# Kernel tuning notes

Measured on AMD Instinct MI355X. Metric: run time of the kernel, lower is better.

## Reference

```python
import jax, jax.numpy as jnp
import numpy as np

HIDDEN = 1024
HEADS = 16
HEAD_DIM = HIDDEN // HEADS
SCALE = float(np.sqrt(HEAD_DIM))


def setup_inputs() -> dict:
    key = jax.random.key(0)
    ks = jax.random.split(key, 9)
    B, S = 2, 2048
    x = jax.random.normal(ks[0], (B, S, HIDDEN), dtype=jnp.float32)
    mask = jnp.ones((B, S, S), dtype=jnp.int32)
    init = 1.0 / np.sqrt(HIDDEN)
    def lin(k):
        kw, kb = jax.random.split(k)
        W = jax.random.uniform(kw, (HIDDEN, HIDDEN), jnp.float32, -init, init)
        b = jax.random.uniform(kb, (HIDDEN,), jnp.float32, -init, init)
        return W, b
    Wq, bq = lin(ks[1])
    Wk, bk = lin(ks[2])
    Wv, bv = lin(ks[3])
    Wo, bo = lin(ks[4])
    return {"x": x, "mask": mask, "Wq": Wq, "bq": bq, "Wk": Wk, "bk": bk,
            "Wv": Wv, "bv": bv, "Wo": Wo, "bo": bo}


def reference(x, mask, Wq, bq, Wk, bk, Wv, bv, Wo, bo):
    B, S, _ = x.shape
    # Linear projections, split into heads: [B, H, S, Dh]
    def proj(W, b):
        y = jnp.einsum('bsd,ed->bse', x, W) + b  # torch Linear: x @ W.T + b
        return y.reshape(B, S, HEADS, HEAD_DIM).transpose(0, 2, 1, 3)
    q = proj(Wq, bq)
    k = proj(Wk, bk)
    v = proj(Wv, bv)
    scores = jnp.einsum('bhqd,bhkd->bhqk', q, k) / SCALE  # [B,H,S,S]
    scores = jnp.where(mask[:, None, :, :] == 0, jnp.float32(-1e9), scores)
    attn = jax.nn.softmax(scores, axis=-1)
    # dropout is identity at inference (eval mode)
    out = jnp.einsum('bhqk,bhkd->bhqd', attn, v)
    out = out.transpose(0, 2, 1, 3).reshape(B, S, HIDDEN)
    return jnp.einsum('bsd,ed->bse', out, Wo) + bo
```

## Files before the change

kernel.cpp:

```cpp
#include <hip/hip_runtime.h>
#include <hip/hip_bf16.h>

typedef __attribute__((ext_vector_type(8))) short bf16x8;
typedef __attribute__((ext_vector_type(4))) float f32x4;
typedef __attribute__((ext_vector_type(16))) float f32x16;
typedef unsigned int uint;

typedef __attribute__((address_space(1))) void as1_void;
typedef __attribute__((address_space(3))) void as3_void;

__device__ __forceinline__ void gload16(const void* g, void* l) {
  __builtin_amdgcn_global_load_lds((as1_void*)(void*)g, (as3_void*)l, 16, 0, 0);
}

__device__ __forceinline__ f32x4 mfma16(bf16x8 a, bf16x8 b, f32x4 c) {
  return __builtin_amdgcn_mfma_f32_16x16x32_bf16(a, b, c, 0, 0, 0);
}

__device__ __forceinline__ f32x16 mfma32(bf16x8 a, bf16x8 b, f32x16 c) {
  return __builtin_amdgcn_mfma_f32_32x32x16_bf16(a, b, c, 0, 0, 0);
}

__global__ __launch_bounds__(256) void castf2b(const float* __restrict__ s,
                                               __hip_bfloat16* __restrict__ d, int n) {
  int i = (blockIdx.x * 256 + threadIdx.x) * 4;
  if (i >= n) return;
  float4 f = *reinterpret_cast<const float4*>(s + i);
  union { __hip_bfloat16 h[4]; uint2 u; } cv;
  cv.h[0] = __float2bfloat16(f.x);
  cv.h[1] = __float2bfloat16(f.y);
  cv.h[2] = __float2bfloat16(f.z);
  cv.h[3] = __float2bfloat16(f.w);
  *reinterpret_cast<uint2*>(d + i) = cv.u;
}

__global__ __launch_bounds__(256) void castw(
    const float* __restrict__ Wq, const float* __restrict__ Wk,
    const float* __restrict__ Wv, const float* __restrict__ Wo,
    __hip_bfloat16* __restrict__ wqkv, __hip_bfloat16* __restrict__ wo) {
  int seg = blockIdx.x >> 10;
  int i = ((blockIdx.x & 1023) * 256 + threadIdx.x) * 4;
  const float* s = seg == 0 ? Wq : seg == 1 ? Wk : seg == 2 ? Wv : Wo;
  __hip_bfloat16* d = seg < 3 ? wqkv + seg * 1048576 : wo;
  float4 f = *reinterpret_cast<const float4*>(s + i);
  union { __hip_bfloat16 h[4]; uint2 u; } cv;
  cv.h[0] = __float2bfloat16(f.x);
  cv.h[1] = __float2bfloat16(f.y);
  cv.h[2] = __float2bfloat16(f.z);
  cv.h[3] = __float2bfloat16(f.w);
  *reinterpret_cast<uint2*>(d + i) = cv.u;
}

__global__ __launch_bounds__(256) void mask_pack(const int* __restrict__ m,
                                                 unsigned long long* __restrict__ bits) {
  int g = blockIdx.x * 256 + threadIdx.x;
  unsigned long long bal = __ballot(m[g] != 0);
  if ((threadIdx.x & 63) == 0) bits[g >> 6] = bal;
}

__global__ __launch_bounds__(256) void vtrans(const __hip_bfloat16* __restrict__ v,
                                              __hip_bfloat16* __restrict__ vt) {
  int bh = blockIdx.x >> 5;
  int s0 = (blockIdx.x & 31) * 64;
  __shared__ __align__(16) __hip_bfloat16 tile[64][72];
  const __hip_bfloat16* src = v + ((size_t)bh * 2048 + s0) * 64;
  int t = threadIdx.x;
#pragma unroll
  for (int i = 0; i < 2; i++) {
    int c = t + i * 256;
    int r = c >> 3, c8 = (c & 7) * 8;
    *reinterpret_cast<uint4*>(&tile[r][c8]) =
        *reinterpret_cast<const uint4*>(src + (size_t)r * 64 + c8);
  }
  __syncthreads();
  __hip_bfloat16* dst = vt + (size_t)bh * 64 * 2048 + s0;
#pragma unroll
  for (int i = 0; i < 2; i++) {
    int c = t + i * 256;
    int d = c >> 3, s8 = (c & 7) * 8;
    __hip_bfloat16 tmp[8] __attribute__((aligned(16)));
#pragma unroll
    for (int j = 0; j < 8; j++) tmp[j] = tile[s8 + j][d];
    *reinterpret_cast<uint4*>(dst + (size_t)d * 2048 + s8) =
        *reinterpret_cast<const uint4*>(tmp);
  }
}

template <int MODE>
__global__ __launch_bounds__(256) void gemm_bt(
    const __hip_bfloat16* __restrict__ A, const __hip_bfloat16* __restrict__ Bw,
    const float* __restrict__ bias0, const float* __restrict__ bias1,
    const float* __restrict__ bias2, __hip_bfloat16* __restrict__ out0,
    __hip_bfloat16* __restrict__ out1, __hip_bfloat16* __restrict__ out2,
    float* __restrict__ foutp, int M, int N, int K) {
  __shared__ __align__(16) __hip_bfloat16 Alds[128 * 64];
  __shared__ __align__(16) __hip_bfloat16 Blds[128 * 64];
  const int t = threadIdx.x;
  const int lane = t & 63;
  const int w = t >> 6;
  const int wr = w >> 1, wc = w & 1;
  const int l15 = lane & 15, lhi = lane >> 4;
  const int Nt = N >> 7;
  const int bm = (int)blockIdx.x / Nt, bn = (int)blockIdx.x % Nt;
  const int m0 = bm * 128, n0 = bn * 128;

  const f32x4 fzero = {0.f, 0.f, 0.f, 0.f};
  f32x4 acc[4][4];
#pragma unroll
  for (int mi = 0; mi < 4; mi++)
#pragma unroll
    for (int ni = 0; ni < 4; ni++) acc[mi][ni] = fzero;

  for (int k0 = 0; k0 < K; k0 += 64) {
#pragma unroll
    for (int i = 0; i < 4; i++) {
      int c = t + i * 256;
      int r = c >> 3, c8 = (c & 7) * 8;
      gload16(A + (size_t)(m0 + r) * K + k0 + c8, (char*)Alds + c * 16);
      gload16(Bw + (size_t)(n0 + r) * K + k0 + c8, (char*)Blds + c * 16);
    }
    __syncthreads();
#pragma unroll
    for (int kk = 0; kk < 2; kk++) {
      bf16x8 af[4], bfr[4];
#pragma unroll
      for (int mi = 0; mi < 4; mi++)
        af[mi] = *reinterpret_cast<const bf16x8*>(
            &Alds[(wr * 64 + mi * 16 + l15) * 64 + kk * 32 + lhi * 8]);
#pragma unroll
      for (int ni = 0; ni < 4; ni++)
        bfr[ni] = *reinterpret_cast<const bf16x8*>(
            &Blds[(wc * 64 + ni * 16 + l15) * 64 + kk * 32 + lhi * 8]);
#pragma unroll
      for (int mi = 0; mi < 4; mi++)
#pragma unroll
        for (int ni = 0; ni < 4; ni++)
          acc[mi][ni] = mfma16(af[mi], bfr[ni], acc[mi][ni]);
    }
    __syncthreads();
  }

#pragma unroll
  for (int mi = 0; mi < 4; mi++) {
#pragma unroll
    for (int ni = 0; ni < 4; ni++) {
#pragma unroll
      for (int r = 0; r < 4; r++) {
        int gr = m0 + wr * 64 + mi * 16 + lhi * 4 + r;
        int gc = n0 + wc * 64 + ni * 16 + l15;
        float v = acc[mi][ni][r];
        if (MODE == 0) {
          int seg = gc >> 10, e = gc & 1023, h = e >> 6, d = e & 63;
          int b = gr >> 11, s = gr & 2047;
          size_t idx = (((size_t)(b * 16 + h)) * 2048 + s) * 64 + d;
          if (seg == 0)
            out0[idx] = __float2bfloat16((v + bias0[e]) * 0.125f);
          else if (seg == 1)
            out1[idx] = __float2bfloat16(v + bias1[e]);
          else
            out2[idx] = __float2bfloat16(v + bias2[e]);
        } else {
          foutp[(size_t)gr * N + gc] = v + bias0[gc];
        }
      }
    }
  }
}

__global__ __launch_bounds__(256) void attn2(
    const __hip_bfloat16* __restrict__ Q, const __hip_bfloat16* __restrict__ Kk,
    const __hip_bfloat16* __restrict__ VT,
    const unsigned long long* __restrict__ mb, __hip_bfloat16* __restrict__ ctx) {
  int bx = blockIdx.x;
  int bid = (bx & 7) * 128 + (bx >> 3);
  int bh = bid >> 5, qc = bid & 31;
  int b = bh >> 4, h = bh & 15;
  int lane = threadIdx.x & 63, w = threadIdx.x >> 6;
  int l31 = lane & 31, lh = lane >> 5, lh4 = lh * 4;
  int wsb = w & 1;
  int kvh = w >> 1;
  int q0 = qc * 64 + wsb * 32;
  int kvbase = kvh * 1024;

  __shared__ float olds[2][32][64];
  __shared__ float mlds[2][2][32];
  __shared__ float llds[2][2][32];

  const __hip_bfloat16* Qrow = Q + ((size_t)bh * 2048 + q0 + l31) * 64 + lh * 8;
  const __hip_bfloat16* Krow =
      Kk + ((size_t)bh * 2048 + kvbase + l31) * 64 + lh * 8;
  const __hip_bfloat16* V0 =
      VT + ((size_t)bh * 64 + l31) * 2048 + kvbase + lh * 8;
  const __hip_bfloat16* V1 = V0 + 32 * 2048;
  const unsigned long long* Mrow =
      mb + ((size_t)b * 2048 + q0 + l31) * 32 + kvh * 16;

  bf16x8 qf[4];
#pragma unroll
  for (int ck = 0; ck < 4; ck++)
    qf[ck] = *reinterpret_cast<const bf16x8*>(Qrow + ck * 16);

  f32x16 o0 = {}, o1 = {};
  float mrun = -3.0e38f, lrun = 0.f;

  unsigned long long mw = Mrow[0], mwn = 0;
  bool skipm = __all(mw == ~0ull);

  auto comp = [&](const bf16x8* kf, const bf16x8* vf, int sh) {
    f32x16 s = {};
#pragma unroll
    for (int ck = 0; ck < 4; ck++) s = mfma32(kf[ck], qf[ck], s);
    if (!skipm) {
      uint mh = (uint)(mw >> sh) >> lh4;
#pragma unroll
      for (int r = 0; r < 16; r++) {
        int cr = (r & 3) + 8 * (r >> 2);
        if (!((mh >> cr) & 1u)) s[r] = -1e9f;
      }
    }
    float pmax = s[0];
#pragma unroll
    for (int r = 1; r < 16; r++) pmax = fmaxf(pmax, s[r]);
    pmax = fmaxf(pmax, __shfl_xor(pmax, 32));
    if (!__all(pmax <= mrun + 8.0f)) {
      float nm = fmaxf(mrun, pmax);
      float scl = __expf(mrun - nm);
      mrun = nm;
      lrun *= scl;
#pragma unroll
      for (int r = 0; r < 16; r++) {
        int cr = (r & 3) + 8 * (r >> 2);
        float sr = __shfl(scl, cr + lh4);
        o0[r] *= sr;
        o1[r] *= sr;
      }
    }
    float p[16];
    float ts = 0.f;
#pragma unroll
    for (int r = 0; r < 16; r++) {
      p[r] = __expf(s[r] - mrun);
      ts += p[r];
    }
    ts += __shfl_xor(ts, 32);
    lrun += ts;
    uint x0, x1, x2, x3, y0, y1, y2, y3;
    asm("v_cvt_pk_bf16_f32 %0, %1, %2" : "=v"(x0) : "v"(p[0]), "v"(p[1]));
    asm("v_cvt_pk_bf16_f32 %0, %1, %2" : "=v"(y0) : "v"(p[4]), "v"(p[5]));
    asm("v_cvt_pk_bf16_f32 %0, %1, %2" : "=v"(x1) : "v"(p[2]), "v"(p[3]));
    asm("v_cvt_pk_bf16_f32 %0, %1, %2" : "=v"(y1) : "v"(p[6]), "v"(p[7]));
    asm("v_cvt_pk_bf16_f32 %0, %1, %2" : "=v"(x2) : "v"(p[8]), "v"(p[9]));
    asm("v_cvt_pk_bf16_f32 %0, %1, %2" : "=v"(y2) : "v"(p[12]), "v"(p[13]));
    asm("v_cvt_pk_bf16_f32 %0, %1, %2" : "=v"(x3) : "v"(p[10]), "v"(p[11]));
    asm("v_cvt_pk_bf16_f32 %0, %1, %2" : "=v"(y3) : "v"(p[14]), "v"(p[15]));
    asm volatile("v_permlane32_swap_b32 %0, %1" : "+v"(x0), "+v"(y0));
    asm volatile("v_permlane32_swap_b32 %0, %1" : "+v"(x1), "+v"(y1));
    asm volatile("v_permlane32_swap_b32 %0, %1" : "+v"(x2), "+v"(y2));
    asm volatile("v_permlane32_swap_b32 %0, %1" : "+v"(x3), "+v"(y3));
    union { uint u[4]; bf16x8 v8; } pa0, pa1;
    pa0.u[0] = x0; pa0.u[1] = x1; pa0.u[2] = y0; pa0.u[3] = y1;
    pa1.u[0] = x2; pa1.u[1] = x3; pa1.u[2] = y2; pa1.u[3] = y3;
    o0 = mfma32(pa0.v8, vf[0], o0);
    o0 = mfma32(pa1.v8, vf[1], o0);
    o1 = mfma32(pa0.v8, vf[2], o1);
    o1 = mfma32(pa1.v8, vf[3], o1);
  };

  bf16x8 kfA[4], vfA[4], kfB[4], vfB[4];
#pragma unroll
  for (int ck = 0; ck < 4; ck++)
    kfA[ck] = *reinterpret_cast<const bf16x8*>(Krow + ck * 16);
  vfA[0] = *reinterpret_cast<const bf16x8*>(V0);
  vfA[1] = *reinterpret_cast<const bf16x8*>(V0 + 16);
  vfA[2] = *reinterpret_cast<const bf16x8*>(V1);
  vfA[3] = *reinterpret_cast<const bf16x8*>(V1 + 16);

  for (int i = 0; i < 16; ++i) {
    const int t1 = 2 * i + 1;
#pragma unroll
    for (int ck = 0; ck < 4; ck++)
      kfB[ck] = *reinterpret_cast<const bf16x8*>(Krow + t1 * 2048 + ck * 16);
    vfB[0] = *reinterpret_cast<const bf16x8*>(V0 + t1 * 32);
    vfB[1] = *reinterpret_cast<const bf16x8*>(V0 + t1 * 32 + 16);
    vfB[2] = *reinterpret_cast<const bf16x8*>(V1 + t1 * 32);
    vfB[3] = *reinterpret_cast<const bf16x8*>(V1 + t1 * 32 + 16);
    mwn = Mrow[i + 1 < 16 ? i + 1 : 15];

    comp(kfA, vfA, 0);

    if (i < 15) {
      const int t2 = 2 * i + 2;
#pragma unroll
      for (int ck = 0; ck < 4; ck++)
        kfA[ck] = *reinterpret_cast<const bf16x8*>(Krow + t2 * 2048 + ck * 16);
      vfA[0] = *reinterpret_cast<const bf16x8*>(V0 + t2 * 32);
      vfA[1] = *reinterpret_cast<const bf16x8*>(V0 + t2 * 32 + 16);
      vfA[2] = *reinterpret_cast<const bf16x8*>(V1 + t2 * 32);
      vfA[3] = *reinterpret_cast<const bf16x8*>(V1 + t2 * 32 + 16);
    }

    comp(kfB, vfB, 32);

    mw = mwn;
    skipm = __all(mw == ~0ull);
  }

  if (lh == 0) {
    mlds[wsb][kvh][l31] = mrun;
    llds[wsb][kvh][l31] = lrun;
  }
  __syncthreads();
  float mA = mlds[wsb][0][l31], mB = mlds[wsb][1][l31];
  float lA = llds[wsb][0][l31], lB = llds[wsb][1][l31];
  float mN = fmaxf(mA, mB);
  float aA = __expf(mA - mN), aB = __expf(mB - mN);
  if (kvh) {
#pragma unroll
    for (int r = 0; r < 16; r++) {
      int cr = (r & 3) + 8 * (r >> 2);
      float ar = __shfl(aB, cr + lh4);
      olds[wsb][r][lane] = o0[r] * ar;
      olds[wsb][16 + r][lane] = o1[r] * ar;
    }
  }
  __syncthreads();
  if (!kvh) {
    float linv = 1.0f / (lA * aA + lB * aB);
    size_t obase = ((size_t)b * 2048 + q0) * 1024 + (size_t)h * 64 + l31;
#pragma unroll
    for (int r = 0; r < 16; r++) {
      int cr = (r & 3) + 8 * (r >> 2);
      int rho = cr + lh4;
      float ar = __shfl(aA, rho);
      float li = __shfl(linv, rho);
      float v0 = o0[r] * ar + olds[wsb][r][lane];
      float v1 = o1[r] * ar + olds[wsb][16 + r][lane];
      ctx[obase + (size_t)rho * 1024] = __float2bfloat16(v0 * li);
      ctx[obase + (size_t)rho * 1024 + 32] = __float2bfloat16(v1 * li);
    }
  }
}

extern "C" void kernel_launch(void* const* d_in, const int* in_sizes, int n_in,
                              void* d_out, int out_size, void* d_ws,
                              size_t ws_size, hipStream_t stream) {
  const float* x = (const float*)d_in[0];
  const int* mask = (const int*)d_in[1];
  const float* Wq = (const float*)d_in[2];
  const float* bq = (const float*)d_in[3];
  const float* Wk = (const float*)d_in[4];
  const float* bk = (const float*)d_in[5];
  const float* Wv = (const float*)d_in[6];
  const float* bv = (const float*)d_in[7];
  const float* Wo = (const float*)d_in[8];
  const float* bo = (const float*)d_in[9];
  float* out = (float*)d_out;
  char* ws = (char*)d_ws;

  __hip_bfloat16* xb   = (__hip_bfloat16*)(ws);
  __hip_bfloat16* wqkv = (__hip_bfloat16*)(ws + 8388608);
  __hip_bfloat16* wo   = (__hip_bfloat16*)(ws + 14680064);
  __hip_bfloat16* qws  = (__hip_bfloat16*)(ws + 16777216);
  __hip_bfloat16* kws  = (__hip_bfloat16*)(ws + 25165824);
  __hip_bfloat16* vtmp = (__hip_bfloat16*)(ws + 33554432);
  __hip_bfloat16* vt   = (__hip_bfloat16*)(ws + 41943040);
  __hip_bfloat16* ctx  = (__hip_bfloat16*)(ws + 50331648);
  unsigned long long* mbits = (unsigned long long*)(ws + 58720256);

  castf2b<<<4096, 256, 0, stream>>>(x, xb, 4194304);
  castw<<<4096, 256, 0, stream>>>(Wq, Wk, Wv, Wo, wqkv, wo);
  mask_pack<<<32768, 256, 0, stream>>>(mask, mbits);

  gemm_bt<0><<<768, 256, 0, stream>>>(xb, wqkv, bq, bk, bv, qws, kws, vtmp,
                                      nullptr, 4096, 3072, 1024);
  vtrans<<<1024, 256, 0, stream>>>(vtmp, vt);
  attn2<<<1024, 256, 0, stream>>>(qws, kws, vt, mbits, ctx);
  gemm_bt<1><<<256, 256, 0, stream>>>(ctx, wo, bo, nullptr, nullptr, nullptr,
                                      nullptr, nullptr, out, 4096, 1024, 1024);
}
```

Before: 346.1 us.

## Stage K/V tiles through double-buffered LDS with async global-to-LDS loads

The attention kernel stops having each wave load its own K and V fragments from global memory into registers. The block now cooperatively copies each 32-row K/V tile for both KV halves into a double-buffered shared-memory area using global_load_lds, so the two waves that use the same KV half share one copy. An occupancy hint is added through launch bounds. The cost is a block-wide barrier every iteration, and the mask word is no longer prefetched one step ahead.

```diff
diff --git a/kernel.cpp b/kernel.cpp
--- a/kernel.cpp
+++ b/kernel.cpp
@@ -167,7 +167,7 @@
   }
 }
 
-__global__ __launch_bounds__(256) void attn2(
+__global__ __launch_bounds__(256, 4) void attn3(
     const __hip_bfloat16* __restrict__ Q, const __hip_bfloat16* __restrict__ Kk,
     const __hip_bfloat16* __restrict__ VT,
     const unsigned long long* __restrict__ mb, __hip_bfloat16* __restrict__ ctx) {
@@ -180,36 +180,78 @@
   int wsb = w & 1;
   int kvh = w >> 1;
   int q0 = qc * 64 + wsb * 32;
-  int kvbase = kvh * 1024;
-
-  __shared__ float olds[2][32][64];
+
+  __shared__ __align__(16) char tiles[2][4][4096];
   __shared__ float mlds[2][2][32];
   __shared__ float llds[2][2][32];
-
-  const __hip_bfloat16* Qrow = Q + ((size_t)bh * 2048 + q0 + l31) * 64 + lh * 8;
-  const __hip_bfloat16* Krow =
-      Kk + ((size_t)bh * 2048 + kvbase + l31) * 64 + lh * 8;
-  const __hip_bfloat16* V0 =
-      VT + ((size_t)bh * 64 + l31) * 2048 + kvbase + lh * 8;
-  const __hip_bfloat16* V1 = V0 + 32 * 2048;
+  float* olds = (float*)&tiles[0][0][0];
+
+  const int t = threadIdx.x;
+  const __hip_bfloat16* Kg = Kk + (size_t)bh * 2048 * 64;
+  const __hip_bfloat16* Vg = VT + (size_t)bh * 64 * 2048;
   const unsigned long long* Mrow =
       mb + ((size_t)b * 2048 + q0 + l31) * 32 + kvh * 16;
 
   bf16x8 qf[4];
-#pragma unroll
-  for (int ck = 0; ck < 4; ck++)
-    qf[ck] = *reinterpret_cast<const bf16x8*>(Qrow + ck * 16);
+  {
+    const __hip_bfloat16* Qrow =
+        Q + ((size_t)bh * 2048 + q0 + l31) * 64 + lh * 8;
+#pragma unroll
+    for (int ck = 0; ck < 4; ck++)
+      qf[ck] = *reinterpret_cast<const bf16x8*>(Qrow + ck * 16);
+  }
+
+  auto stage = [&](int buf, int kvt) {
+    {
+      int r = t & 31, s = t >> 5;
+      gload16(Kg + (size_t)(kvt * 32 + r) * 64 + s * 8,
+              &tiles[buf][0][t * 16]);
+      gload16(Kg + (size_t)(1024 + kvt * 32 + r) * 64 + s * 8,
+              &tiles[buf][1][t * 16]);
+    }
+    {
+      int r = t & 63, s = t >> 6;
+      gload16(Vg + (size_t)r * 2048 + kvt * 32 + s * 8,
+              &tiles[buf][2][t * 16]);
+      gload16(Vg + (size_t)r * 2048 + 1024 + kvt * 32 + s * 8,
+              &tiles[buf][3][t * 16]);
+    }
+  };
 
   f32x16 o0 = {}, o1 = {};
   float mrun = -3.0e38f, lrun = 0.f;
 
-  unsigned long long mw = Mrow[0], mwn = 0;
-  bool skipm = __all(mw == ~0ull);
-
-  auto comp = [&](const bf16x8* kf, const bf16x8* vf, int sh) {
+  stage(0, 0);
+  __syncthreads();
+
+  unsigned long long mw = ~0ull;
+  bool skipm = true;
+
+  for (int i = 0; i < 32; ++i) {
+    const int cur = i & 1;
+    if (i < 31) stage(cur ^ 1, i + 1);
+    if ((i & 1) == 0) {
+      mw = Mrow[i >> 1];
+      skipm = __all(mw == ~0ull);
+    }
+    const int sh = (i & 1) * 32;
+
+    const bf16x8* kb = (const bf16x8*)&tiles[cur][kvh][0];
+    const bf16x8* vb = (const bf16x8*)&tiles[cur][2 + kvh][0];
+
     f32x16 s = {};
-#pragma unroll
-    for (int ck = 0; ck < 4; ck++) s = mfma32(kf[ck], qf[ck], s);
+    {
+      bf16x8 kf[4];
+#pragma unroll
+      for (int ck = 0; ck < 4; ck++) kf[ck] = kb[(ck * 2 + lh) * 32 + l31];
+#pragma unroll
+      for (int ck = 0; ck < 4; ck++) s = mfma32(kf[ck], qf[ck], s);
+    }
+    bf16x8 vf[4];
+#pragma unroll
+    for (int j = 0; j < 4; j++)
+      vf[j] = vb[((j & 1) * 2 + lh) * 64 + (j >> 1) * 32 + l31];
+
     if (!skipm) {
       uint mh = (uint)(mw >> sh) >> lh4;
 #pragma unroll
@@ -264,45 +306,8 @@
     o0 = mfma32(pa1.v8, vf[1], o0);
     o1 = mfma32(pa0.v8, vf[2], o1);
     o1 = mfma32(pa1.v8, vf[3], o1);
-  };
-
-  bf16x8 kfA[4], vfA[4], kfB[4], vfB[4];
-#pragma unroll
-  for (int ck = 0; ck < 4; ck++)
-    kfA[ck] = *reinterpret_cast<const bf16x8*>(Krow + ck * 16);
-  vfA[0] = *reinterpret_cast<const bf16x8*>(V0);
-  vfA[1] = *reinterpret_cast<const bf16x8*>(V0 + 16);
-  vfA[2] = *reinterpret_cast<const bf16x8*>(V1);
-  vfA[3] = *reinterpret_cast<const bf16x8*>(V1 + 16);
-
-  for (int i = 0; i < 16; ++i) {
-    const int t1 = 2 * i + 1;
-#pragma unroll
-    for (int ck = 0; ck < 4; ck++)
-      kfB[ck] = *reinterpret_cast<const bf16x8*>(Krow + t1 * 2048 + ck * 16);
-    vfB[0] = *reinterpret_cast<const bf16x8*>(V0 + t1 * 32);
-    vfB[1] = *reinterpret_cast<const bf16x8*>(V0 + t1 * 32 + 16);
-    vfB[2] = *reinterpret_cast<const bf16x8*>(V1 + t1 * 32);
-    vfB[3] = *reinterpret_cast<const bf16x8*>(V1 + t1 * 32 + 16);
-    mwn = Mrow[i + 1 < 16 ? i + 1 : 15];
-
-    comp(kfA, vfA, 0);
-
-    if (i < 15) {
-      const int t2 = 2 * i + 2;
-#pragma unroll
-      for (int ck = 0; ck < 4; ck++)
-        kfA[ck] = *reinterpret_cast<const bf16x8*>(Krow + t2 * 2048 + ck * 16);
-      vfA[0] = *reinterpret_cast<const bf16x8*>(V0 + t2 * 32);
-      vfA[1] = *reinterpret_cast<const bf16x8*>(V0 + t2 * 32 + 16);
-      vfA[2] = *reinterpret_cast<const bf16x8*>(V1 + t2 * 32);
-      vfA[3] = *reinterpret_cast<const bf16x8*>(V1 + t2 * 32 + 16);
-    }
-
-    comp(kfB, vfB, 32);
-
-    mw = mwn;
-    skipm = __all(mw == ~0ull);
+
+    __syncthreads();
   }
 
   if (lh == 0) {
@@ -319,8 +324,8 @@
     for (int r = 0; r < 16; r++) {
       int cr = (r & 3) + 8 * (r >> 2);
       float ar = __shfl(aB, cr + lh4);
-      olds[wsb][r][lane] = o0[r] * ar;
-      olds[wsb][16 + r][lane] = o1[r] * ar;
+      olds[(wsb * 32 + r) * 64 + lane] = o0[r] * ar;
+      olds[(wsb * 32 + 16 + r) * 64 + lane] = o1[r] * ar;
     }
   }
   __syncthreads();
@@ -333,8 +338,8 @@
       int rho = cr + lh4;
       float ar = __shfl(aA, rho);
       float li = __shfl(linv, rho);
-      float v0 = o0[r] * ar + olds[wsb][r][lane];
-      float v1 = o1[r] * ar + olds[wsb][16 + r][lane];
+      float v0 = o0[r] * ar + olds[(wsb * 32 + r) * 64 + lane];
+      float v1 = o1[r] * ar + olds[(wsb * 32 + 16 + r) * 64 + lane];
       ctx[obase + (size_t)rho * 1024] = __float2bfloat16(v0 * li);
       ctx[obase + (size_t)rho * 1024 + 32] = __float2bfloat16(v1 * li);
     }
@@ -374,7 +379,7 @@
   gemm_bt<0><<<768, 256, 0, stream>>>(xb, wqkv, bq, bk, bv, qws, kws, vtmp,
                                       nullptr, 4096, 3072, 1024);
   vtrans<<<1024, 256, 0, stream>>>(vtmp, vt);
-  attn2<<<1024, 256, 0, stream>>>(qws, kws, vt, mbits, ctx);
+  attn3<<<1024, 256, 0, stream>>>(qws, kws, vt, mbits, ctx);
   gemm_bt<1><<<256, 256, 0, stream>>>(ctx, wo, bo, nullptr, nullptr, nullptr,
                                       nullptr, nullptr, out, 4096, 1024, 1024);
 }
```

After: 300.3 us. 1.15x faster.
